# Kernel tuning notes

Hardware: AMD Instinct MI355X
Metric: run time of the kernel (lower is better)

## Reference

```python
import jax, jax.numpy as jnp
import numpy as np

N_NODES = 20000
N_EDGES = 640000
MUL = 32      # multiplicity of the 0e and 1o node-feature irreps
ATTR = 8      # node attr scalars (0e)
RBASIS = 16   # radial edge embedding size (0e)
FC_HID = 64   # radial MLP hidden size
AVG_NEIGH = 32.0
LOG2 = 0.6931471805599453


def _ssp(x):
    # ShiftedSoftPlus: softplus(x) - log(2)
    return jax.nn.softplus(x) - LOG2


def setup_inputs() -> dict:
    key = jax.random.key(0)
    ks = jax.random.split(key, 16)
    return {
        "node_s": jax.random.normal(ks[0], (N_NODES, MUL), jnp.float32),
        "node_v": jax.random.normal(ks[1], (N_NODES, MUL, 3), jnp.float32),
        "node_attrs": jax.random.uniform(ks[2], (N_NODES, ATTR), dtype=jnp.float32),
        "edge_emb": jax.random.normal(ks[3], (N_EDGES, RBASIS), jnp.float32),
        "edge_y0": jnp.ones((N_EDGES, 1), jnp.float32),  # Y_0 spherical harmonic is constant
        "edge_y1": jax.random.normal(ks[4], (N_EDGES, 3), jnp.float32),
        "edge_index": jax.random.randint(ks[5], (2, N_EDGES), 0, N_NODES, jnp.int32),
        "W1s": jax.random.normal(ks[6], (MUL, MUL), jnp.float32),
        "W1v": jax.random.normal(ks[7], (MUL, MUL), jnp.float32),
        "Wr1": jax.random.normal(ks[8], (RBASIS, FC_HID), jnp.float32),
        "Wr2": jax.random.normal(ks[9], (FC_HID, 4 * MUL), jnp.float32),
        "W2s": jax.random.normal(ks[10], (2 * MUL, MUL), jnp.float32),
        "W2v": jax.random.normal(ks[11], (2 * MUL, MUL), jnp.float32),
        "Wscs": jax.random.normal(ks[12], (MUL, ATTR, MUL), jnp.float32),
        "Wscv": jax.random.normal(ks[13], (MUL, ATTR, MUL), jnp.float32),
    }


def reference(node_s, node_v, node_attrs, edge_emb, edge_y0, edge_y1, edge_index,
              W1s, W1v, Wr1, Wr2, W2s, W2v, Wscs, Wscv):
    n = node_s.shape[0]
    src, dst = edge_index[0], edge_index[1]

    # linear_1 (e3nn Linear: per-irrep channel mixing, / sqrt(fan_in))
    inv_m = 1.0 / jnp.sqrt(jnp.float32(MUL))
    s = (node_s @ W1s) * inv_m                              # [N, MUL] 0e
    v = jnp.einsum('nui,uw->nwi', node_v, W1v) * inv_m      # [N, MUL, 3] 1o

    # radial MLP -> per-edge tensor-product weights (4 paths x MUL)
    h = _ssp((edge_emb @ Wr1) / jnp.sqrt(jnp.float32(RBASIS)))
    w = (h @ Wr2) / jnp.sqrt(jnp.float32(FC_HID))           # [E, 4*MUL]
    w1, w2, w3, w4 = jnp.split(w, 4, axis=1)

    # gather source node features
    se = s[src]                                             # [E, MUL]
    ve = v[src]                                             # [E, MUL, 3]

    # CG 'uvu' tensor product (sorted mid irreps: 0e(0ex0e), 0e(1ox1o), 1o(0ex1o), 1o(1ox0e))
    inv_sqrt3 = 1.0 / jnp.sqrt(3.0)
    mid_s = jnp.concatenate([
        w1 * se * edge_y0,                                          # 0e x 0e -> 0e
        w4 * jnp.einsum('eui,ei->eu', ve, edge_y1) * inv_sqrt3,     # 1o x 1o -> 0e
    ], axis=1)                                              # [E, 2*MUL]
    mid_v = jnp.concatenate([
        (w2 * se)[:, :, None] * edge_y1[:, None, :],                # 0e x 1o -> 1o
        w3[:, :, None] * ve * edge_y0[:, :, None],                  # 1o x 0e -> 1o
    ], axis=1)                                              # [E, 2*MUL, 3]

    # scatter-sum to destination nodes, / sqrt(avg_num_neighbors)
    inv_deg = 1.0 / jnp.sqrt(jnp.float32(AVG_NEIGH))
    agg_s = jax.ops.segment_sum(mid_s, dst, num_segments=n) * inv_deg
    agg_v = jax.ops.segment_sum(mid_v, dst, num_segments=n) * inv_deg

    # linear_2
    inv_2m = 1.0 / jnp.sqrt(jnp.float32(2 * MUL))
    ns = (agg_s @ W2s) * inv_2m
    nv = jnp.einsum('nui,uw->nwi', agg_v, W2v) * inv_2m

    # self connection: FullyConnectedTensorProduct(node_feats_in, node_attrs)
    inv_fan = 1.0 / jnp.sqrt(jnp.float32(MUL * ATTR))
    sc_s = jnp.einsum('nu,nv,uvw->nw', node_s, node_attrs, Wscs) * inv_fan
    sc_v = jnp.einsum('nui,nv,uvw->nwi', node_v, node_attrs, Wscv) * inv_fan

    out_s = ns + sc_s                                       # [N, MUL]
    out_v = (nv + sc_v).reshape(n, 3 * MUL)                 # [N, 3*MUL]
    return jnp.concatenate([out_s, out_v], axis=1)          # [N, 4*MUL] flat irreps layout
```

## Files before the change

kernel.cpp:

```cpp
#include <hip/hip_runtime.h>
#include <math.h>

typedef short bf16x8 __attribute__((ext_vector_type(8)));
typedef short short2v __attribute__((ext_vector_type(2)));
typedef float f32x4 __attribute__((ext_vector_type(4)));

__device__ __forceinline__ float sspf(float x) {
    return __logf(1.0f + __expf(x)) - 0.6931471805599453f;
}
__device__ __forceinline__ short f2b(float f) {
    union { float f; unsigned u; } c; c.f = f;
    unsigned r = c.u + 0x7fff + ((c.u >> 16) & 1);
    return (short)(r >> 16);
}
__device__ __forceinline__ float b2f(short s) {
    union { unsigned u; float f; } c; c.u = ((unsigned)(unsigned short)s) << 16;
    return c.f;
}
__device__ __forceinline__ int rlanei(int v, int l) {
    return __builtin_amdgcn_readlane(v, l);
}
__device__ __forceinline__ float rlanef(float v, int l) {
    return __uint_as_float(__builtin_amdgcn_readlane(__float_as_uint(v), l));
}
__device__ __forceinline__ bf16x8 pack8(float4 a, float4 b) {
    bf16x8 o;
    o[0] = f2b(a.x); o[1] = f2b(a.y); o[2] = f2b(a.z); o[3] = f2b(a.w);
    o[4] = f2b(b.x); o[5] = f2b(b.y); o[6] = f2b(b.z); o[7] = f2b(b.w);
    return o;
}

constexpr float INV_M      = 0.17677669529663687f;
constexpr float INV_R      = 0.25f;
constexpr float INV_H      = 0.125f;
constexpr float INV_2M_DEG = 0.125f * 0.17677669529663687f;
constexpr float INV_FAN    = 0.0625f;
constexpr float INV_SQRT3  = 0.5773502691896258f;

__global__ __launch_bounds__(256) void k_lin1h(
    const float* __restrict__ node_s, const float* __restrict__ node_v,
    const float* __restrict__ W1s, const float* __restrict__ W1v,
    float* __restrict__ s_ws, float* __restrict__ v_ws, int N,
    const int* __restrict__ eidx, int* __restrict__ count, int E,
    float4* __restrict__ aggz, int nagg4, int nblin, int nbhist)
{
    int b = blockIdx.x;
    int tid = threadIdx.x;
    if (b >= nblin + nbhist) {
        int i0 = (b - nblin - nbhist) * 1024 + tid;
        #pragma unroll
        for (int r = 0; r < 4; ++r) {
            int idx = i0 + r * 256;
            if (idx < nagg4) aggz[idx] = make_float4(0.f, 0.f, 0.f, 0.f);
        }
        return;
    }
    if (b >= nblin) {
        int e = (b - nblin) * 256 + tid;
        if (e < E) atomicAdd(&count[eidx[E + e]], 1);
        return;
    }
    __shared__ short sF[4 * 512];
    {
        int f = tid >> 6, ln = tid & 63;
        int q = ln >> 4, lm = ln & 15;
        int nt = f & 1;
        const float* Wp = (f < 2) ? W1s : W1v;
        short* d8 = &sF[tid * 8];
        #pragma unroll
        for (int j = 0; j < 8; ++j) {
            int k = q * 8 + j;
            d8[j] = f2b(Wp[k * 32 + nt * 16 + lm] * INV_M);
        }
    }
    __syncthreads();
    int lane = tid & 63, wv = tid >> 6;
    int q = lane >> 4, lm = lane & 15;
    int n0 = (b * 4 + wv) * 16;
    if (n0 >= N) return;
    int nr = n0 + lm;

    const float* nsp = node_s + (size_t)nr * 32;
    bf16x8 as8 = pack8(*(const float4*)(nsp + q * 8), *(const float4*)(nsp + q * 8 + 4));
    #pragma unroll
    for (int nt = 0; nt < 2; ++nt) {
        bf16x8 bfr = *(const bf16x8*)&sF[(nt * 64 + lane) * 8];
        f32x4 acc = __builtin_amdgcn_mfma_f32_16x16x32_bf16(
            as8, bfr, (f32x4){0.f, 0.f, 0.f, 0.f}, 0, 0, 0);
        #pragma unroll
        for (int r = 0; r < 4; ++r)
            s_ws[(size_t)(n0 + q * 4 + r) * 32 + nt * 16 + lm] = acc[r];
    }
    const float* nvp = node_v + (size_t)nr * 96;
    #pragma unroll
    for (int i = 0; i < 3; ++i) {
        bf16x8 av8;
        #pragma unroll
        for (int j = 0; j < 8; ++j) av8[j] = f2b(nvp[(q * 8 + j) * 3 + i]);
        #pragma unroll
        for (int nt = 0; nt < 2; ++nt) {
            bf16x8 bfr = *(const bf16x8*)&sF[((2 + nt) * 64 + lane) * 8];
            f32x4 acc = __builtin_amdgcn_mfma_f32_16x16x32_bf16(
                av8, bfr, (f32x4){0.f, 0.f, 0.f, 0.f}, 0, 0, 0);
            #pragma unroll
            for (int r = 0; r < 4; ++r)
                v_ws[(size_t)(n0 + q * 4 + r) * 96 + i * 32 + nt * 16 + lm] = acc[r];
        }
    }
}

__global__ __launch_bounds__(1024) void k_scan(
    const int* __restrict__ count, int* __restrict__ cursor, int N)
{
    __shared__ int wsum[16], woff[16];
    int tid = threadIdx.x;
    int per = (N + 1023) / 1024;
    int base = tid * per;
    int lim = min(N, base + per);
    int s = 0;
    for (int i = base; i < lim; ++i) s += count[i];
    int lane = tid & 63, wv = tid >> 6;
    int x = s;
    #pragma unroll
    for (int off = 1; off < 64; off <<= 1) {
        int y = __shfl_up(x, off, 64);
        if (lane >= off) x += y;
    }
    if (lane == 63) wsum[wv] = x;
    __syncthreads();
    if (wv == 0 && lane < 16) {
        int t = wsum[lane];
        int xx = t;
        #pragma unroll
        for (int off = 1; off < 16; off <<= 1) {
            int y = __shfl_up(xx, off, 64);
            if (lane >= off) xx += y;
        }
        woff[lane] = xx - t;
    }
    __syncthreads();
    int run = x - s + woff[wv];
    for (int i = base; i < lim; ++i) {
        int c = count[i];
        cursor[i] = run;
        run += c;
    }
}

__global__ __launch_bounds__(256) void k_fill(
    const int* __restrict__ eidx, int* __restrict__ cursor,
    int2* __restrict__ epair, int E)
{
    int e = blockIdx.x * 256 + threadIdx.x;
    if (e < E) {
        int d = eidx[E + e];
        int slot = atomicAdd(&cursor[d], 1);
        epair[slot] = make_int2(e, d);
    }
}

__global__ __launch_bounds__(256) void k_fused(
    const float* __restrict__ emb, const int2* __restrict__ epair,
    const int* __restrict__ eidx, const float* __restrict__ y0v,
    const float* __restrict__ y1,
    const float* __restrict__ Wr1, const float* __restrict__ Wr2,
    const float* __restrict__ s_ws, const float* __restrict__ v_ws,
    float* __restrict__ agg_s, float* __restrict__ agg_v, int E)
{
    __shared__ short sW1[4 * 512];
    __shared__ short hbuf[4][16 * 72];
    __shared__ short wtl[4][2 * 64 * 18];

    int tid = threadIdx.x;
    {
        int f = tid >> 6, ln = tid & 63;
        int qq = ln >> 4, lmm = ln & 15;
        short* d8 = &sW1[(f * 64 + ln) * 8];
        #pragma unroll
        for (int j = 0; j < 8; ++j) {
            int k = qq * 8 + j;
            d8[j] = (k < 16) ? f2b(Wr1[k * 64 + f * 16 + lmm] * INV_R) : (short)0;
        }
    }
    __syncthreads();

    int lane = tid & 63, wv = tid >> 6;
    int q = lane >> 4, lm = lane & 15;
    int u = lane & 31;
    bool low = (lane < 32);

    bf16x8 wr2f[16];
    #pragma unroll
    for (int nt = 0; nt < 8; ++nt) {
        #pragma unroll
        for (int kc = 0; kc < 2; ++kc) {
            #pragma unroll
            for (int j = 0; j < 8; ++j) {
                int k = kc * 32 + q * 8 + j;
                wr2f[nt * 2 + kc][j] = f2b(Wr2[k * 128 + nt * 16 + lm] * INV_H);
            }
        }
    }

    short* hl = hbuf[wv];
    short* wl = wtl[wv];

    int base = blockIdx.x * 256 + wv * 64;
    if (base >= E) return;

    int2 nep = epair[min(base + lm, E - 1)];
    float4 pa = make_float4(0.f, 0.f, 0.f, 0.f);
    float4 pb = make_float4(0.f, 0.f, 0.f, 0.f);
    if (q < 2) {
        const float* ep = emb + (size_t)nep.x * 16 + q * 8;
        pa = *(const float4*)ep;
        pb = *(const float4*)(ep + 4);
    }

    float accs = 0.f, acc0 = 0.f, acc1 = 0.f, acc2 = 0.f;
    int cur = -1;

    for (int ch = 0; ch < 4; ++ch) {
        int cb = base + ch * 16;
        int2 myep = nep;

        int srcv = 0;
        if (lane >= 16 && lane < 32) srcv = eidx[myep.x];
        int meta = (lane < 16) ? myep.y : srcv;
        float pkm = (q < 3) ? y1[(size_t)myep.x * 3 + q] : y0v[myep.x];

        bf16x8 af = (bf16x8){0, 0, 0, 0, 0, 0, 0, 0};
        if (q < 2) af = pack8(pa, pb);
        if (ch < 3) {
            nep = epair[min(cb + 16 + lm, E - 1)];
            if (q < 2) {
                const float* ep = emb + (size_t)nep.x * 16 + q * 8;
                pa = *(const float4*)ep;
                pb = *(const float4*)(ep + 4);
            }
        }

        #pragma unroll
        for (int nt = 0; nt < 4; ++nt) {
            bf16x8 bfr = *(const bf16x8*)&sW1[(nt * 64 + lane) * 8];
            f32x4 x = __builtin_amdgcn_mfma_f32_16x16x32_bf16(
                af, bfr, (f32x4){0.f, 0.f, 0.f, 0.f}, 0, 0, 0);
            #pragma unroll
            for (int r = 0; r < 4; ++r)
                hl[(q * 4 + r) * 72 + nt * 16 + lm] = f2b(sspf(x[r]));
        }

        bf16x8 ha = *(const bf16x8*)&hl[lm * 72 + q * 8];
        bf16x8 hb = *(const bf16x8*)&hl[lm * 72 + 32 + q * 8];
        #pragma unroll
        for (int nt = 0; nt < 8; ++nt) {
            f32x4 acc = __builtin_amdgcn_mfma_f32_16x16x32_bf16(
                ha, wr2f[nt * 2], (f32x4){0.f, 0.f, 0.f, 0.f}, 0, 0, 0);
            acc = __builtin_amdgcn_mfma_f32_16x16x32_bf16(hb, wr2f[nt * 2 + 1], acc, 0, 0, 0);
            int cp = (nt & 1) * 16 + lm + ((nt >> 2) & 1) * 32;
            int half = (nt >> 1) & 1;
            short* wp = &wl[half * 1152 + cp * 18 + q * 4];
            short2v p01 = {f2b(acc[0]), f2b(acc[1])};
            short2v p23 = {f2b(acc[2]), f2b(acc[3])};
            *(short2v*)&wp[0] = p01;
            *(short2v*)&wp[2] = p23;
        }

        float pse[4], pvx[4], pvy[4], pvz[4];
        #pragma unroll
        for (int k = 0; k < 4; ++k) {
            int sr = rlanei(meta, 16 + k);
            const float* sp = s_ws + (size_t)sr * 32;
            const float* vp = v_ws + (size_t)sr * 96;
            pse[k] = sp[u]; pvx[k] = vp[u]; pvy[k] = vp[32 + u]; pvz[k] = vp[64 + u];
        }
        #pragma unroll
        for (int i = 0; i < 16; ++i) {
            float se = pse[i & 3], vx = pvx[i & 3], vy = pvy[i & 3], vz = pvz[i & 3];
            if (i + 4 < 16) {
                int sr = rlanei(meta, 16 + i + 4);
                const float* sp = s_ws + (size_t)sr * 32;
                const float* vp = v_ws + (size_t)sr * 96;
                pse[(i + 4) & 3] = sp[u]; pvx[(i + 4) & 3] = vp[u];
                pvy[(i + 4) & 3] = vp[32 + u]; pvz[(i + 4) & 3] = vp[64 + u];
            }
            int d = rlanei(meta, i);
            if (d != cur) {
                if (cur >= 0) {
                    atomicAdd(&agg_s[(size_t)cur * 64 + lane], accs);
                    float* av = &agg_v[(size_t)cur * 192 + lane];
                    atomicAdd(av, acc0); atomicAdd(av + 64, acc1); atomicAdd(av + 128, acc2);
                }
                accs = acc0 = acc1 = acc2 = 0.f;
                cur = d;
            }
            float la = b2f(wl[lane * 18 + i]);
            float lb = b2f(wl[1152 + lane * 18 + i]);
            float y1x = rlanef(pkm, i);
            float y1y = rlanef(pkm, 16 + i);
            float y1z = rlanef(pkm, 32 + i);
            float y0e = rlanef(pkm, 48 + i);
            float dot = vx * y1x + vy * y1y + vz * y1z;
            accs += low ? (la * se * y0e) : (lb * dot * INV_SQRT3);
            float t = low ? (lb * se) : (la * y0e);
            acc0 = fmaf(t, low ? y1x : vx, acc0);
            acc1 = fmaf(t, low ? y1y : vy, acc1);
            acc2 = fmaf(t, low ? y1z : vz, acc2);
        }
    }
    if (cur >= 0) {
        atomicAdd(&agg_s[(size_t)cur * 64 + lane], accs);
        float* av = &agg_v[(size_t)cur * 192 + lane];
        atomicAdd(av, acc0); atomicAdd(av + 64, acc1); atomicAdd(av + 128, acc2);
    }
}

__global__ __launch_bounds__(256) void k_out(
    const float* __restrict__ node_s, const float* __restrict__ node_v,
    const float* __restrict__ attrs,
    const float* __restrict__ agg_s, const float* __restrict__ agg_v,
    const float* __restrict__ W2s, const float* __restrict__ W2v,
    const float* __restrict__ Wscs, const float* __restrict__ Wscv,
    float* __restrict__ out, int N)
{
    __shared__ short sB[40 * 512];
    int tid = threadIdx.x;
    for (int idx = tid; idx < 20480; idx += 256) {
        int f = idx >> 9, r = idx & 511;
        int ln = r >> 3, j = r & 7;
        int qq = ln >> 4, lmm = ln & 15;
        const float* Wp; int nt, t; float sc;
        if (f < 4)       { Wp = W2s;  nt = f >> 1;              t = f & 1; sc = INV_2M_DEG; }
        else if (f < 8)  { int g = f - 4;  Wp = W2v;  nt = g >> 1; t = g & 1; sc = INV_2M_DEG; }
        else if (f < 24) { int g = f - 8;  Wp = Wscs; nt = g >> 3; t = g & 7; sc = INV_FAN; }
        else             { int g = f - 24; Wp = Wscv; nt = g >> 3; t = g & 7; sc = INV_FAN; }
        sB[idx] = f2b(Wp[(t * 32 + qq * 8 + j) * 32 + nt * 16 + lmm] * sc);
    }
    __syncthreads();

    int lane = tid & 63, wv = tid >> 6;
    int q = lane >> 4, lm = lane & 15;
    int n0 = (blockIdx.x * 4 + wv) * 16;
    if (n0 >= N) return;
    int nr = n0 + lm;

    float4 at0 = *(const float4*)(attrs + (size_t)nr * 8);
    float4 at1 = *(const float4*)(attrs + (size_t)nr * 8 + 4);
    float at[8] = {at0.x, at0.y, at0.z, at0.w, at1.x, at1.y, at1.z, at1.w};

    const float* asp = agg_s + (size_t)nr * 64;
    bf16x8 aS[2];
    #pragma unroll
    for (int kc = 0; kc < 2; ++kc)
        aS[kc] = pack8(*(const float4*)(asp + kc * 32 + q * 8),
                       *(const float4*)(asp + kc * 32 + q * 8 + 4));

    const float* nsp = node_s + (size_t)nr * 32;
    bf16x8 scs[8];
    #pragma unroll
    for (int t = 0; t < 8; ++t) {
        float nv_ = nsp[t * 4 + q];
        #pragma unroll
        for (int j = 0; j < 8; ++j) scs[t][j] = f2b(nv_ * at[j]);
    }

    #pragma unroll
    for (int nt = 0; nt < 2; ++nt) {
        f32x4 acc = (f32x4){0.f, 0.f, 0.f, 0.f};
        acc = __builtin_amdgcn_mfma_f32_16x16x32_bf16(
            aS[0], *(const bf16x8*)&sB[(nt * 2 + 0) * 512 + lane * 8], acc, 0, 0, 0);
        acc = __builtin_amdgcn_mfma_f32_16x16x32_bf16(
            aS[1], *(const bf16x8*)&sB[(nt * 2 + 1) * 512 + lane * 8], acc, 0, 0, 0);
        #pragma unroll
        for (int t = 0; t < 8; ++t)
            acc = __builtin_amdgcn_mfma_f32_16x16x32_bf16(
                scs[t], *(const bf16x8*)&sB[(8 + nt * 8 + t) * 512 + lane * 8], acc, 0, 0, 0);
        #pragma unroll
        for (int r = 0; r < 4; ++r)
            out[(size_t)(n0 + q * 4 + r) * 128 + nt * 16 + lm] = acc[r];
    }

    const float* nvp = node_v + (size_t)nr * 96;
    const float* avp = agg_v + (size_t)nr * 192;
    #pragma unroll
    for (int i = 0; i < 3; ++i) {
        bf16x8 aV[2];
        #pragma unroll
        for (int kc = 0; kc < 2; ++kc)
            aV[kc] = pack8(*(const float4*)(avp + i * 64 + kc * 32 + q * 8),
                           *(const float4*)(avp + i * 64 + kc * 32 + q * 8 + 4));
        bf16x8 scv[8];
        #pragma unroll
        for (int t = 0; t < 8; ++t) {
            float nv_ = nvp[(t * 4 + q) * 3 + i];
            #pragma unroll
            for (int j = 0; j < 8; ++j) scv[t][j] = f2b(nv_ * at[j]);
        }
        #pragma unroll
        for (int nt = 0; nt < 2; ++nt) {
            f32x4 acc = (f32x4){0.f, 0.f, 0.f, 0.f};
            acc = __builtin_amdgcn_mfma_f32_16x16x32_bf16(
                aV[0], *(const bf16x8*)&sB[(4 + nt * 2 + 0) * 512 + lane * 8], acc, 0, 0, 0);
            acc = __builtin_amdgcn_mfma_f32_16x16x32_bf16(
                aV[1], *(const bf16x8*)&sB[(4 + nt * 2 + 1) * 512 + lane * 8], acc, 0, 0, 0);
            #pragma unroll
            for (int t = 0; t < 8; ++t)
                acc = __builtin_amdgcn_mfma_f32_16x16x32_bf16(
                    scv[t], *(const bf16x8*)&sB[(24 + nt * 8 + t) * 512 + lane * 8], acc, 0, 0, 0);
            #pragma unroll
            for (int r = 0; r < 4; ++r)
                out[(size_t)(n0 + q * 4 + r) * 128 + 32 + (nt * 16 + lm) * 3 + i] = acc[r];
        }
    }
}

extern "C" void kernel_launch(void* const* d_in, const int* in_sizes, int n_in,
                              void* d_out, int out_size, void* d_ws, size_t ws_size,
                              hipStream_t stream)
{
    const float* node_s = (const float*)d_in[0];
    const float* node_v = (const float*)d_in[1];
    const float* attrs  = (const float*)d_in[2];
    const float* emb    = (const float*)d_in[3];
    const float* y0     = (const float*)d_in[4];
    const float* y1     = (const float*)d_in[5];
    const int*   eidx   = (const int*)d_in[6];
    const float* W1s  = (const float*)d_in[7];
    const float* W1v  = (const float*)d_in[8];
    const float* Wr1  = (const float*)d_in[9];
    const float* Wr2  = (const float*)d_in[10];
    const float* W2s  = (const float*)d_in[11];
    const float* W2v  = (const float*)d_in[12];
    const float* Wscs = (const float*)d_in[13];
    const float* Wscv = (const float*)d_in[14];

    int N = in_sizes[0] / 32;
    int E = in_sizes[3] / 16;

    float* s_ws  = (float*)d_ws;
    float* v_ws  = s_ws + (size_t)N * 32;
    float* agg_s = v_ws + (size_t)N * 96;
    float* agg_v = agg_s + (size_t)N * 64;
    int* count   = (int*)(agg_v + (size_t)N * 192);
    int* cursor  = count + N;
    int2* epair  = (int2*)(cursor + N);

    hipMemsetAsync(count, 0, (size_t)N * sizeof(int), stream);

    int nblin  = (N + 63) / 64;
    int nbhist = (E + 255) / 256;
    int nagg4  = N * 64;
    int nbz    = (nagg4 + 1023) / 1024;
    k_lin1h<<<dim3(nblin + nbhist + nbz), dim3(256), 0, stream>>>(
        node_s, node_v, W1s, W1v, s_ws, v_ws, N,
        eidx, count, E, (float4*)agg_s, nagg4, nblin, nbhist);
    k_scan<<<dim3(1), dim3(1024), 0, stream>>>(count, cursor, N);
    k_fill<<<dim3((E + 255) / 256), dim3(256), 0, stream>>>(eidx, cursor, epair, E);
    k_fused<<<dim3((E + 255) / 256), dim3(256), 0, stream>>>(emb, epair, eidx, y0, y1,
                                                             Wr1, Wr2, s_ws, v_ws,
                                                             agg_s, agg_v, E);
    k_out<<<dim3((N + 63) / 64), dim3(256), 0, stream>>>(node_s, node_v, attrs, agg_s, agg_v,
                                                         W2s, W2v, Wscs, Wscv, (float*)d_out, N);
}
```

Measured before the change: 376.6 us.

## Pack linear_1 node features as interleaved bf16 for single-load gathers

The linear_1 outputs (scalar plus three vector components per channel) are now stored as one interleaved bf16 record per node and channel instead of two separate fp32 arrays. The edge kernel gathers each source node's features with a single 8-byte load rather than four scattered 4-byte loads. This cuts gather traffic and the number of memory transactions in the hot fused edge kernel. The cost is lower precision on the gathered features, since they are rounded to bf16 before the products.

New measurement: 371.9 us. No clear change (-1.3%).

```diff
diff --git a/kernel.cpp b/kernel.cpp
--- a/kernel.cpp
+++ b/kernel.cpp
@@ -3,6 +3,7 @@
 
 typedef short bf16x8 __attribute__((ext_vector_type(8)));
 typedef short short2v __attribute__((ext_vector_type(2)));
+typedef short short4v __attribute__((ext_vector_type(4)));
 typedef float f32x4 __attribute__((ext_vector_type(4)));
 
 __device__ __forceinline__ float sspf(float x) {
@@ -40,7 +41,7 @@
 __global__ __launch_bounds__(256) void k_lin1h(
     const float* __restrict__ node_s, const float* __restrict__ node_v,
     const float* __restrict__ W1s, const float* __restrict__ W1v,
-    float* __restrict__ s_ws, float* __restrict__ v_ws, int N,
+    short* __restrict__ feat, int N,
     const int* __restrict__ eidx, int* __restrict__ count, int E,
     float4* __restrict__ aggz, int nagg4, int nblin, int nbhist)
 {
@@ -82,29 +83,29 @@
 
     const float* nsp = node_s + (size_t)nr * 32;
     bf16x8 as8 = pack8(*(const float4*)(nsp + q * 8), *(const float4*)(nsp + q * 8 + 4));
+    const float* nvp = node_v + (size_t)nr * 96;
+    bf16x8 av8[3];
+    #pragma unroll
+    for (int i = 0; i < 3; ++i)
+        #pragma unroll
+        for (int j = 0; j < 8; ++j) av8[i][j] = f2b(nvp[(q * 8 + j) * 3 + i]);
+
     #pragma unroll
     for (int nt = 0; nt < 2; ++nt) {
-        bf16x8 bfr = *(const bf16x8*)&sF[(nt * 64 + lane) * 8];
-        f32x4 acc = __builtin_amdgcn_mfma_f32_16x16x32_bf16(
-            as8, bfr, (f32x4){0.f, 0.f, 0.f, 0.f}, 0, 0, 0);
-        #pragma unroll
-        for (int r = 0; r < 4; ++r)
-            s_ws[(size_t)(n0 + q * 4 + r) * 32 + nt * 16 + lm] = acc[r];
-    }
-    const float* nvp = node_v + (size_t)nr * 96;
-    #pragma unroll
-    for (int i = 0; i < 3; ++i) {
-        bf16x8 av8;
-        #pragma unroll
-        for (int j = 0; j < 8; ++j) av8[j] = f2b(nvp[(q * 8 + j) * 3 + i]);
-        #pragma unroll
-        for (int nt = 0; nt < 2; ++nt) {
-            bf16x8 bfr = *(const bf16x8*)&sF[((2 + nt) * 64 + lane) * 8];
-            f32x4 acc = __builtin_amdgcn_mfma_f32_16x16x32_bf16(
-                av8, bfr, (f32x4){0.f, 0.f, 0.f, 0.f}, 0, 0, 0);
-            #pragma unroll
-            for (int r = 0; r < 4; ++r)
-                v_ws[(size_t)(n0 + q * 4 + r) * 96 + i * 32 + nt * 16 + lm] = acc[r];
+        bf16x8 bs = *(const bf16x8*)&sF[(nt * 64 + lane) * 8];
+        bf16x8 bv = *(const bf16x8*)&sF[((2 + nt) * 64 + lane) * 8];
+        f32x4 sa = __builtin_amdgcn_mfma_f32_16x16x32_bf16(
+            as8, bs, (f32x4){0.f, 0.f, 0.f, 0.f}, 0, 0, 0);
+        f32x4 v0 = __builtin_amdgcn_mfma_f32_16x16x32_bf16(
+            av8[0], bv, (f32x4){0.f, 0.f, 0.f, 0.f}, 0, 0, 0);
+        f32x4 v1 = __builtin_amdgcn_mfma_f32_16x16x32_bf16(
+            av8[1], bv, (f32x4){0.f, 0.f, 0.f, 0.f}, 0, 0, 0);
+        f32x4 v2 = __builtin_amdgcn_mfma_f32_16x16x32_bf16(
+            av8[2], bv, (f32x4){0.f, 0.f, 0.f, 0.f}, 0, 0, 0);
+        #pragma unroll
+        for (int r = 0; r < 4; ++r) {
+            short4v o = {f2b(sa[r]), f2b(v0[r]), f2b(v1[r]), f2b(v2[r])};
+            *(short4v*)&feat[(size_t)(n0 + q * 4 + r) * 128 + (nt * 16 + lm) * 4] = o;
         }
     }
 }
@@ -164,7 +165,7 @@
     const int* __restrict__ eidx, const float* __restrict__ y0v,
     const float* __restrict__ y1,
     const float* __restrict__ Wr1, const float* __restrict__ Wr2,
-    const float* __restrict__ s_ws, const float* __restrict__ v_ws,
+    const short* __restrict__ feat,
     float* __restrict__ agg_s, float* __restrict__ agg_v, int E)
 {
     __shared__ short sW1[4 * 512];
@@ -266,24 +267,20 @@
             *(short2v*)&wp[2] = p23;
         }
 
-        float pse[4], pvx[4], pvy[4], pvz[4];
+        short4v pg[4];
         #pragma unroll
         for (int k = 0; k < 4; ++k) {
             int sr = rlanei(meta, 16 + k);
-            const float* sp = s_ws + (size_t)sr * 32;
-            const float* vp = v_ws + (size_t)sr * 96;
-            pse[k] = sp[u]; pvx[k] = vp[u]; pvy[k] = vp[32 + u]; pvz[k] = vp[64 + u];
+            pg[k] = *(const short4v*)&feat[(size_t)sr * 128 + u * 4];
         }
         #pragma unroll
         for (int i = 0; i < 16; ++i) {
-            float se = pse[i & 3], vx = pvx[i & 3], vy = pvy[i & 3], vz = pvz[i & 3];
+            short4v g = pg[i & 3];
             if (i + 4 < 16) {
                 int sr = rlanei(meta, 16 + i + 4);
-                const float* sp = s_ws + (size_t)sr * 32;
-                const float* vp = v_ws + (size_t)sr * 96;
-                pse[(i + 4) & 3] = sp[u]; pvx[(i + 4) & 3] = vp[u];
-                pvy[(i + 4) & 3] = vp[32 + u]; pvz[(i + 4) & 3] = vp[64 + u];
+                pg[(i + 4) & 3] = *(const short4v*)&feat[(size_t)sr * 128 + u * 4];
             }
+            float se = b2f(g[0]), vx = b2f(g[1]), vy = b2f(g[2]), vz = b2f(g[3]);
             int d = rlanei(meta, i);
             if (d != cur) {
                 if (cur >= 0) {
@@ -437,11 +434,10 @@
     int N = in_sizes[0] / 32;
     int E = in_sizes[3] / 16;
 
-    float* s_ws  = (float*)d_ws;
-    float* v_ws  = s_ws + (size_t)N * 32;
-    float* agg_s = v_ws + (size_t)N * 96;
+    float* agg_s = (float*)d_ws;
     float* agg_v = agg_s + (size_t)N * 64;
-    int* count   = (int*)(agg_v + (size_t)N * 192);
+    short* feat  = (short*)(agg_v + (size_t)N * 192);
+    int* count   = (int*)(feat + (size_t)N * 128);
     int* cursor  = count + N;
     int2* epair  = (int2*)(cursor + N);
 
@@ -452,12 +448,12 @@
     int nagg4  = N * 64;
     int nbz    = (nagg4 + 1023) / 1024;
     k_lin1h<<<dim3(nblin + nbhist + nbz), dim3(256), 0, stream>>>(
-        node_s, node_v, W1s, W1v, s_ws, v_ws, N,
+        node_s, node_v, W1s, W1v, feat, N,
         eidx, count, E, (float4*)agg_s, nagg4, nblin, nbhist);
     k_scan<<<dim3(1), dim3(1024), 0, stream>>>(count, cursor, N);
     k_fill<<<dim3((E + 255) / 256), dim3(256), 0, stream>>>(eidx, cursor, epair, E);
     k_fused<<<dim3((E + 255) / 256), dim3(256), 0, stream>>>(emb, epair, eidx, y0, y1,
-                                                             Wr1, Wr2, s_ws, v_ws,
+                                                             Wr1, Wr2, feat,
                                                              agg_s, agg_v, E);
     k_out<<<dim3((N + 63) / 64), dim3(256), 0, stream>>>(node_s, node_v, attrs, agg_s, agg_v,
                                                          W2s, W2v, Wscs, Wscv, (float*)d_out, N);
```
